# Kernel tuning notes

Measured on AMD Instinct MI355X. Metric: run time of the kernel, lower is better.

Reference implementation:

```python
import jax, jax.numpy as jnp
import numpy as np

CONTEXT_LENGTH = 4096
INPUT_LENGTH = 1024
N_EMBED = 512
HEAD_SIZE = 64
BATCH = 8


def _prefix_causal_mask(T):
    # A=ones(IL,IL), B=zeros(IL,non), C=ones(non,IL), D=tril(non,non)
    il = INPUT_LENGTH
    non = CONTEXT_LENGTH - il
    top = jnp.concatenate([jnp.ones((il, il)), jnp.zeros((il, non))], axis=1)
    bot = jnp.concatenate([jnp.ones((non, il)), jnp.tril(jnp.ones((non, non)))], axis=1)
    E = jnp.concatenate([top, bot], axis=0)
    return E[:T, :T]


def setup_inputs() -> dict:
    key = jax.random.key(0)
    kx, kq, kk, kv = jax.random.split(key, 4)
    scale = N_EMBED ** -0.5
    return {
        "x": jax.random.normal(kx, (BATCH, CONTEXT_LENGTH, N_EMBED), dtype=jnp.float32),
        "Wq": jax.random.normal(kq, (N_EMBED, HEAD_SIZE), dtype=jnp.float32) * scale,
        "Wk": jax.random.normal(kk, (N_EMBED, HEAD_SIZE), dtype=jnp.float32) * scale,
        "Wv": jax.random.normal(kv, (N_EMBED, HEAD_SIZE), dtype=jnp.float32) * scale,
    }


def reference(x, Wq, Wk, Wv):
    B, T, C = x.shape
    q = x @ Wq  # [B,T,h]
    k = x @ Wk  # [B,T,h]
    v = x @ Wv  # [B,T,h]
    # NOTE: original scales by C**-0.5 with C = n_embed (not head_size)
    wei = jnp.einsum("bth,bsh->bts", q, k) * (C ** -0.5)  # [B,T,T]
    mask = _prefix_causal_mask(T)  # [T,T], 1 = visible
    wei = jnp.where(mask == 0, jnp.float32(-jnp.inf), wei)
    wei = jax.nn.softmax(wei, axis=-1)
    # dropout p=0.0 (eval): identity
    return jnp.einsum("bts,bsh->bth", wei, v)  # [B,T,h]
```

## Files before the change

kernel.cpp:

```cpp
#include <hip/hip_runtime.h>
#include <hip/hip_bf16.h>


typedef short short8 __attribute__((ext_vector_type(8)));
typedef float floatx4 __attribute__((ext_vector_type(4)));

static __device__ __forceinline__ unsigned short f2b(float f) {
  unsigned u = __float_as_uint(f);
  unsigned r = (u + 0x7fffu + ((u >> 16) & 1u)) >> 16;
  return (unsigned short)r;
}

static __device__ __forceinline__ unsigned pkbf(float lo, float hi) {
  __hip_bfloat162 t = __float22bfloat162_rn(make_float2(lo, hi));
  unsigned d;
  __builtin_memcpy(&d, &t, 4);
  return d;
}

union S8U {
  short8 s;
  unsigned u[4];
};

__global__ __launch_bounds__(256) void wtrans(
    const float* __restrict__ Wq, const float* __restrict__ Wk,
    const float* __restrict__ Wv, unsigned short* __restrict__ Wtf) {
  int o = blockIdx.x * 256 + threadIdx.x;
  int e = o & 7;
  int ln = (o >> 3) & 63;
  int jg = o >> 9;
  int ks = jg / 12;
  int j = jg % 12;
  int m = j >> 2;
  int n = (j & 3) * 16 + (ln & 15);
  int k = ks * 32 + (ln >> 4) * 8 + e;
  const float* W = (m == 0) ? Wq : (m == 1) ? Wk : Wv;
  Wtf[o] = f2b(W[k * 64 + n]);
}

__global__ __launch_bounds__(256, 3) void proj(
    const float* __restrict__ x, const unsigned short* __restrict__ Wtf,
    unsigned short* __restrict__ q, unsigned short* __restrict__ Kf,
    unsigned short* __restrict__ Vf) {
  __shared__ float Cc[2][12][16][17];

  const int tid = threadIdx.x;
  const int lane = tid & 63;
  const int w = tid >> 6;
  const int u = lane & 15;
  const int qd = lane >> 4;
  const int pr = w >> 1;
  const int p = w & 1;
  const int g0 = blockIdx.x * 32;

  floatx4 acc[12];
#pragma unroll
  for (int j = 0; j < 12; ++j) acc[j] = (floatx4)0.0f;

  const float* xr = x + (size_t)(g0 + pr * 16 + u) * 512;

  for (int it = 0; it < 8; ++it) {
    const int ks = p + it * 2;
    floatx4 x0 = *reinterpret_cast<const floatx4*>(&xr[ks * 32 + qd * 8]);
    floatx4 x1 = *reinterpret_cast<const floatx4*>(&xr[ks * 32 + qd * 8 + 4]);
    S8U a;
    a.u[0] = pkbf(x0[0], x0[1]);
    a.u[1] = pkbf(x0[2], x0[3]);
    a.u[2] = pkbf(x1[0], x1[1]);
    a.u[3] = pkbf(x1[2], x1[3]);
#pragma unroll
    for (int j = 0; j < 12; ++j) {
      short8 bfr = *reinterpret_cast<const short8*>(&Wtf[(size_t)(ks * 12 + j) * 512 + lane * 8]);
      acc[j] = __builtin_amdgcn_mfma_f32_16x16x32_bf16(a.s, bfr, acc[j], 0, 0, 0);
    }
  }

  if (p == 1) {
#pragma unroll
    for (int j = 0; j < 12; ++j)
#pragma unroll
      for (int r = 0; r < 4; ++r)
        Cc[pr][j][qd * 4 + r][u] = acc[j][r];
  }
  __syncthreads();
  if (p == 0) {
#pragma unroll
    for (int j = 0; j < 12; ++j)
#pragma unroll
      for (int r = 0; r < 4; ++r)
        acc[j][r] += Cc[pr][j][qd * 4 + r][u];

    const int rbase = g0 + pr * 16;
    const int b = rbase >> 12;
    const int t = rbase & 4095;
    const int kt = t >> 6;
    const int sb = ((blockIdx.x & 1) << 1) + pr;
    const int sp = blockIdx.x & 1;
    unsigned short* kfb = Kf + ((size_t)(b * 64 + kt)) * 4096;
    unsigned short* vfb = Vf + ((size_t)(b * 64 + kt)) * 4096;

#pragma unroll
    for (int j = 0; j < 4; ++j)
#pragma unroll
      for (int r = 0; r < 4; ++r) {
        q[(size_t)(rbase + qd * 4 + r) * 64 + j * 16 + u] = f2b(acc[j][r]);
        {
          int kh = j >> 1;
          int qd_f = ((j & 1) << 1) + (u >> 3);
          kfb[(size_t)(kh * 4 + sb) * 512 + (qd_f * 16 + (qd * 4 + r)) * 8 + (u & 7)] =
              f2b(acc[4 + j][r]);
        }
        {
          int qd_f = pr * 2 + (qd >> 1);
          int e = ((qd & 1) << 2) + r;
          vfb[(size_t)(sp * 4 + j) * 512 + (qd_f * 16 + u) * 8 + e] = f2b(acc[8 + j][r]);
        }
      }
  }
}

__global__ __launch_bounds__(256, 2) void attn(
    const unsigned short* __restrict__ q, const unsigned short* __restrict__ Kf,
    const unsigned short* __restrict__ Vf, float* __restrict__ out) {
  __shared__ unsigned Pb[4][4][64][4];
  __shared__ float OcA[64][68];
  __shared__ float OcB[64][68];
  __shared__ float Lc[4][64];

  const int tid = threadIdx.x;
  const int lane = tid & 63;
  const int w = tid >> 6;
  const int u = lane & 15;
  const int qd = lane >> 4;

  const int bx = blockIdx.x;
  const int b = bx & 7;
  const int i = bx >> 3;
  const int qt = (i < 32) ? i : (95 - i);
  const int g0 = qt * 64;

  const unsigned short* qp = q + (size_t)b * 4096 * 64;
  const unsigned short* kfp = Kf + (size_t)b * 64 * 4096;
  const unsigned short* vfp = Vf + (size_t)b * 64 * 4096;

  short8 qB[4][2];
#pragma unroll
  for (int nb = 0; nb < 4; ++nb)
#pragma unroll
    for (int kh = 0; kh < 2; ++kh)
      qB[nb][kh] = *reinterpret_cast<const short8*>(
          &qp[(size_t)(g0 + nb * 16 + u) * 64 + kh * 32 + qd * 8]);

  floatx4 OT[4][4];
#pragma unroll
  for (int mb = 0; mb < 4; ++mb)
#pragma unroll
    for (int nb = 0; nb < 4; ++nb) OT[mb][nb] = (floatx4)0.0f;
  float L[4] = {0.f, 0.f, 0.f, 0.f};

  const float cexp = 0.04419417382415922f * 1.4426950408889634f;
  const int ktmax = (qt < 16) ? 15 : qt;

  for (int kt = w; kt <= ktmax; kt += 4) {
    const unsigned short* kb = kfp + (size_t)kt * 4096;
    const unsigned short* vb = vfp + (size_t)kt * 4096;
    short8 kA[8];
#pragma unroll
    for (int f = 0; f < 8; ++f)
      kA[f] = *reinterpret_cast<const short8*>(&kb[(size_t)f * 512 + lane * 8]);
    const bool diag = (qt >= 16) && (kt == qt);

#pragma unroll
    for (int sp = 0; sp < 2; ++sp) {
      short8 vA[4];
#pragma unroll
      for (int mb = 0; mb < 4; ++mb)
        vA[mb] = *reinterpret_cast<const short8*>(
            &vb[(size_t)(sp * 4 + mb) * 512 + lane * 8]);

      floatx4 ST[2][4];
#pragma unroll
      for (int sbb = 0; sbb < 2; ++sbb)
#pragma unroll
        for (int nb = 0; nb < 4; ++nb) ST[sbb][nb] = (floatx4)0.0f;
#pragma unroll
      for (int kh = 0; kh < 2; ++kh)
#pragma unroll
        for (int sbb = 0; sbb < 2; ++sbb)
#pragma unroll
          for (int nb = 0; nb < 4; ++nb)
            ST[sbb][nb] = __builtin_amdgcn_mfma_f32_16x16x32_bf16(
                kA[kh * 4 + sp * 2 + sbb], qB[nb][kh], ST[sbb][nb], 0, 0, 0);

      if (diag) {
#pragma unroll
        for (int sbb = 0; sbb < 2; ++sbb)
#pragma unroll
          for (int nb = 0; nb < 4; ++nb)
#pragma unroll
            for (int r = 0; r < 4; ++r) {
              int sl = (sp * 2 + sbb) * 16 + qd * 4 + r;
              int qr = nb * 16 + u;
              if (sl > qr) ST[sbb][nb][r] = -__builtin_inff();
            }
      }

#pragma unroll
      for (int sbb = 0; sbb < 2; ++sbb)
#pragma unroll
        for (int nb = 0; nb < 4; ++nb) {
#pragma unroll
          for (int r = 0; r < 4; ++r)
            ST[sbb][nb][r] = __builtin_amdgcn_exp2f(ST[sbb][nb][r] * cexp);
          L[nb] += (ST[sbb][nb][0] + ST[sbb][nb][1]) + (ST[sbb][nb][2] + ST[sbb][nb][3]);
          unsigned lo = pkbf(ST[sbb][nb][0], ST[sbb][nb][1]);
          unsigned hi = pkbf(ST[sbb][nb][2], ST[sbb][nb][3]);
          int dl = (sbb * 2 + (qd >> 1)) * 16 + u;
          int d0 = (qd & 1) * 2;
          *reinterpret_cast<uint2*>(&Pb[w][nb][dl][d0]) = make_uint2(lo, hi);
        }

#pragma unroll
      for (int nb = 0; nb < 4; ++nb) {
        short8 pB = *reinterpret_cast<const short8*>(&Pb[w][nb][lane][0]);
#pragma unroll
        for (int mb = 0; mb < 4; ++mb)
          OT[mb][nb] = __builtin_amdgcn_mfma_f32_16x16x32_bf16(vA[mb], pB, OT[mb][nb], 0, 0, 0);
      }
    }
  }

#pragma unroll
  for (int nb = 0; nb < 4; ++nb) {
    L[nb] += __shfl_xor(L[nb], 16);
    L[nb] += __shfl_xor(L[nb], 32);
  }
  if (lane < 16) {
#pragma unroll
    for (int nb = 0; nb < 4; ++nb) Lc[w][nb * 16 + lane] = L[nb];
  }

  if (w == 1) {
#pragma unroll
    for (int mb = 0; mb < 4; ++mb)
#pragma unroll
      for (int nb = 0; nb < 4; ++nb)
        *reinterpret_cast<floatx4*>(&OcA[nb * 16 + u][mb * 16 + qd * 4]) = OT[mb][nb];
  }
  if (w == 3) {
#pragma unroll
    for (int mb = 0; mb < 4; ++mb)
#pragma unroll
      for (int nb = 0; nb < 4; ++nb)
        *reinterpret_cast<floatx4*>(&OcB[nb * 16 + u][mb * 16 + qd * 4]) = OT[mb][nb];
  }
  __syncthreads();
  if (w == 0) {
#pragma unroll
    for (int mb = 0; mb < 4; ++mb)
#pragma unroll
      for (int nb = 0; nb < 4; ++nb)
        OT[mb][nb] += *reinterpret_cast<const floatx4*>(&OcA[nb * 16 + u][mb * 16 + qd * 4]);
  }
  if (w == 2) {
#pragma unroll
    for (int mb = 0; mb < 4; ++mb)
#pragma unroll
      for (int nb = 0; nb < 4; ++nb) {
        OT[mb][nb] += *reinterpret_cast<const floatx4*>(&OcB[nb * 16 + u][mb * 16 + qd * 4]);
        *reinterpret_cast<floatx4*>(&OcB[nb * 16 + u][mb * 16 + qd * 4]) = OT[mb][nb];
      }
  }
  __syncthreads();
  if (w == 0) {
#pragma unroll
    for (int mb = 0; mb < 4; ++mb)
#pragma unroll
      for (int nb = 0; nb < 4; ++nb) {
        OT[mb][nb] += *reinterpret_cast<const floatx4*>(&OcB[nb * 16 + u][mb * 16 + qd * 4]);
        *reinterpret_cast<floatx4*>(&OcA[nb * 16 + u][mb * 16 + qd * 4]) = OT[mb][nb];
      }
  }
  __syncthreads();

  {
    int qr = tid >> 2;
    int h0 = (tid & 3) * 16;
    float Ltot = (Lc[0][qr] + Lc[1][qr]) + (Lc[2][qr] + Lc[3][qr]);
    float inv = 1.0f / Ltot;
    float* op = out + ((size_t)b * 4096 + g0 + qr) * 64 + h0;
#pragma unroll
    for (int c = 0; c < 4; ++c) {
      floatx4 v = *reinterpret_cast<const floatx4*>(&OcA[qr][h0 + c * 4]);
      v *= inv;
      *reinterpret_cast<floatx4*>(&op[c * 4]) = v;
    }
  }
}

extern "C" void kernel_launch(void* const* d_in, const int* in_sizes, int n_in,
                              void* d_out, int out_size, void* d_ws, size_t ws_size,
                              hipStream_t stream) {
  const float* x  = (const float*)d_in[0];
  const float* Wq = (const float*)d_in[1];
  const float* Wk = (const float*)d_in[2];
  const float* Wv = (const float*)d_in[3];

  unsigned short* ws = (unsigned short*)d_ws;
  unsigned short* Wtf = ws;
  unsigned short* qb = ws + 131072;
  unsigned short* kf = qb + 2097152;
  unsigned short* vf = kf + 2097152;

  wtrans<<<384, 256, 0, stream>>>(Wq, Wk, Wv, Wtf);
  proj<<<1024, 256, 0, stream>>>(x, Wtf, qb, kf, vf);
  attn<<<512, 256, 0, stream>>>(qb, kf, vf, (float*)d_out);
}
```

Baseline: 146.8 us.

## Double-buffer K/V register loads in attention and fold softmax scale into Q

The attention loop now prefetches the next K and V tiles into a second register set while computing on the current one, so global-load latency overlaps the MFMA work. The softmax scale and log2e factor are folded into Q at projection time, which removes a multiply per score. The projection kernel also issues all x loads up front before the MFMA loop. The extra register buffers raise VGPR pressure and may lower occupancy under the launch bounds of 2 blocks per SM. Rounding Q after scaling also changes the bf16 values slightly.

```diff
diff --git a/kernel.cpp b/kernel.cpp
--- a/kernel.cpp
+++ b/kernel.cpp
@@ -54,21 +54,28 @@
   const int p = w & 1;
   const int g0 = blockIdx.x * 32;
 
-  floatx4 acc[12];
-#pragma unroll
-  for (int j = 0; j < 12; ++j) acc[j] = (floatx4)0.0f;
-
   const float* xr = x + (size_t)(g0 + pr * 16 + u) * 512;
 
+  floatx4 xv[16];
+#pragma unroll
   for (int it = 0; it < 8; ++it) {
     const int ks = p + it * 2;
-    floatx4 x0 = *reinterpret_cast<const floatx4*>(&xr[ks * 32 + qd * 8]);
-    floatx4 x1 = *reinterpret_cast<const floatx4*>(&xr[ks * 32 + qd * 8 + 4]);
+    xv[it * 2] = *reinterpret_cast<const floatx4*>(&xr[ks * 32 + qd * 8]);
+    xv[it * 2 + 1] = *reinterpret_cast<const floatx4*>(&xr[ks * 32 + qd * 8 + 4]);
+  }
+
+  floatx4 acc[12];
+#pragma unroll
+  for (int j = 0; j < 12; ++j) acc[j] = (floatx4)0.0f;
+
+#pragma unroll
+  for (int it = 0; it < 8; ++it) {
+    const int ks = p + it * 2;
     S8U a;
-    a.u[0] = pkbf(x0[0], x0[1]);
-    a.u[1] = pkbf(x0[2], x0[3]);
-    a.u[2] = pkbf(x1[0], x1[1]);
-    a.u[3] = pkbf(x1[2], x1[3]);
+    a.u[0] = pkbf(xv[it * 2][0], xv[it * 2][1]);
+    a.u[1] = pkbf(xv[it * 2][2], xv[it * 2][3]);
+    a.u[2] = pkbf(xv[it * 2 + 1][0], xv[it * 2 + 1][1]);
+    a.u[3] = pkbf(xv[it * 2 + 1][2], xv[it * 2 + 1][3]);
 #pragma unroll
     for (int j = 0; j < 12; ++j) {
       short8 bfr = *reinterpret_cast<const short8*>(&Wtf[(size_t)(ks * 12 + j) * 512 + lane * 8]);
@@ -91,6 +98,7 @@
       for (int r = 0; r < 4; ++r)
         acc[j][r] += Cc[pr][j][qd * 4 + r][u];
 
+    const float cexp = 0.04419417382415922f * 1.4426950408889634f;
     const int rbase = g0 + pr * 16;
     const int b = rbase >> 12;
     const int t = rbase & 4095;
@@ -104,7 +112,7 @@
     for (int j = 0; j < 4; ++j)
 #pragma unroll
       for (int r = 0; r < 4; ++r) {
-        q[(size_t)(rbase + qd * 4 + r) * 64 + j * 16 + u] = f2b(acc[j][r]);
+        q[(size_t)(rbase + qd * 4 + r) * 64 + j * 16 + u] = f2b(acc[j][r] * cexp);
         {
           int kh = j >> 1;
           int qd_f = ((j & 1) << 1) + (u >> 3);
@@ -159,77 +167,101 @@
     for (int nb = 0; nb < 4; ++nb) OT[mb][nb] = (floatx4)0.0f;
   float L[4] = {0.f, 0.f, 0.f, 0.f};
 
-  const float cexp = 0.04419417382415922f * 1.4426950408889634f;
   const int ktmax = (qt < 16) ? 15 : qt;
 
-  for (int kt = w; kt <= ktmax; kt += 4) {
-    const unsigned short* kb = kfp + (size_t)kt * 4096;
-    const unsigned short* vb = vfp + (size_t)kt * 4096;
-    short8 kA[8];
-#pragma unroll
-    for (int f = 0; f < 8; ++f)
-      kA[f] = *reinterpret_cast<const short8*>(&kb[(size_t)f * 512 + lane * 8]);
-    const bool diag = (qt >= 16) && (kt == qt);
-
-#pragma unroll
-    for (int sp = 0; sp < 2; ++sp) {
-      short8 vA[4];
-#pragma unroll
-      for (int mb = 0; mb < 4; ++mb)
-        vA[mb] = *reinterpret_cast<const short8*>(
-            &vb[(size_t)(sp * 4 + mb) * 512 + lane * 8]);
-
-      floatx4 ST[2][4];
-#pragma unroll
-      for (int sbb = 0; sbb < 2; ++sbb)
-#pragma unroll
-        for (int nb = 0; nb < 4; ++nb) ST[sbb][nb] = (floatx4)0.0f;
-#pragma unroll
-      for (int kh = 0; kh < 2; ++kh)
-#pragma unroll
-        for (int sbb = 0; sbb < 2; ++sbb)
-#pragma unroll
-          for (int nb = 0; nb < 4; ++nb)
-            ST[sbb][nb] = __builtin_amdgcn_mfma_f32_16x16x32_bf16(
-                kA[kh * 4 + sp * 2 + sbb], qB[nb][kh], ST[sbb][nb], 0, 0, 0);
-
-      if (diag) {
-#pragma unroll
-        for (int sbb = 0; sbb < 2; ++sbb)
-#pragma unroll
-          for (int nb = 0; nb < 4; ++nb)
-#pragma unroll
-            for (int r = 0; r < 4; ++r) {
-              int sl = (sp * 2 + sbb) * 16 + qd * 4 + r;
-              int qr = nb * 16 + u;
-              if (sl > qr) ST[sbb][nb][r] = -__builtin_inff();
-            }
-      }
-
-#pragma unroll
-      for (int sbb = 0; sbb < 2; ++sbb)
-#pragma unroll
-        for (int nb = 0; nb < 4; ++nb) {
-#pragma unroll
-          for (int r = 0; r < 4; ++r)
-            ST[sbb][nb][r] = __builtin_amdgcn_exp2f(ST[sbb][nb][r] * cexp);
-          L[nb] += (ST[sbb][nb][0] + ST[sbb][nb][1]) + (ST[sbb][nb][2] + ST[sbb][nb][3]);
-          unsigned lo = pkbf(ST[sbb][nb][0], ST[sbb][nb][1]);
-          unsigned hi = pkbf(ST[sbb][nb][2], ST[sbb][nb][3]);
-          int dl = (sbb * 2 + (qd >> 1)) * 16 + u;
-          int d0 = (qd & 1) * 2;
-          *reinterpret_cast<uint2*>(&Pb[w][nb][dl][d0]) = make_uint2(lo, hi);
-        }
-
-#pragma unroll
-      for (int nb = 0; nb < 4; ++nb) {
-        short8 pB = *reinterpret_cast<const short8*>(&Pb[w][nb][lane][0]);
-#pragma unroll
-        for (int mb = 0; mb < 4; ++mb)
-          OT[mb][nb] = __builtin_amdgcn_mfma_f32_16x16x32_bf16(vA[mb], pB, OT[mb][nb], 0, 0, 0);
-      }
+#define LOADKV(KA, VA, KT)                                                    \
+  do {                                                                        \
+    const unsigned short* kb_ = kfp + (size_t)(KT) * 4096;                    \
+    const unsigned short* vb_ = vfp + (size_t)(KT) * 4096;                    \
+    _Pragma("unroll")                                                         \
+    for (int f = 0; f < 8; ++f) {                                             \
+      KA[f] = *reinterpret_cast<const short8*>(&kb_[(size_t)f * 512 + lane * 8]); \
+      VA[f] = *reinterpret_cast<const short8*>(&vb_[(size_t)f * 512 + lane * 8]); \
+    }                                                                         \
+  } while (0)
+
+#define ATTN_STEP(KA, VA, KT)                                                 \
+  do {                                                                        \
+    const bool diag_ = (qt >= 16) && ((KT) == qt);                            \
+    _Pragma("unroll")                                                         \
+    for (int sp = 0; sp < 2; ++sp) {                                          \
+      floatx4 ST[2][4];                                                       \
+      _Pragma("unroll")                                                       \
+      for (int sbb = 0; sbb < 2; ++sbb)                                       \
+        _Pragma("unroll")                                                     \
+        for (int nb = 0; nb < 4; ++nb) ST[sbb][nb] = (floatx4)0.0f;           \
+      _Pragma("unroll")                                                       \
+      for (int kh = 0; kh < 2; ++kh)                                          \
+        _Pragma("unroll")                                                     \
+        for (int sbb = 0; sbb < 2; ++sbb)                                     \
+          _Pragma("unroll")                                                   \
+          for (int nb = 0; nb < 4; ++nb)                                      \
+            ST[sbb][nb] = __builtin_amdgcn_mfma_f32_16x16x32_bf16(            \
+                KA[kh * 4 + sp * 2 + sbb], qB[nb][kh], ST[sbb][nb], 0, 0, 0); \
+      if (diag_) {                                                            \
+        _Pragma("unroll")                                                     \
+        for (int sbb = 0; sbb < 2; ++sbb)                                     \
+          _Pragma("unroll")                                                   \
+          for (int nb = 0; nb < 4; ++nb)                                      \
+            _Pragma("unroll")                                                 \
+            for (int r = 0; r < 4; ++r) {                                     \
+              int sl = (sp * 2 + sbb) * 16 + qd * 4 + r;                      \
+              int qr = nb * 16 + u;                                           \
+              if (sl > qr) ST[sbb][nb][r] = -__builtin_inff();                \
+            }                                                                 \
+      }                                                                       \
+      _Pragma("unroll")                                                       \
+      for (int sbb = 0; sbb < 2; ++sbb)                                       \
+        _Pragma("unroll")                                                     \
+        for (int nb = 0; nb < 4; ++nb) {                                      \
+          _Pragma("unroll")                                                   \
+          for (int r = 0; r < 4; ++r)                                         \
+            ST[sbb][nb][r] = __builtin_amdgcn_exp2f(ST[sbb][nb][r]);          \
+          L[nb] += (ST[sbb][nb][0] + ST[sbb][nb][1]) +                        \
+                   (ST[sbb][nb][2] + ST[sbb][nb][3]);                         \
+          unsigned lo = pkbf(ST[sbb][nb][0], ST[sbb][nb][1]);                 \
+          unsigned hi = pkbf(ST[sbb][nb][2], ST[sbb][nb][3]);                 \
+          int dl = (sbb * 2 + (qd >> 1)) * 16 + u;                            \
+          int d0 = (qd & 1) * 2;                                              \
+          *reinterpret_cast<uint2*>(&Pb[w][nb][dl][d0]) = make_uint2(lo, hi); \
+        }                                                                     \
+      _Pragma("unroll")                                                       \
+      for (int nb = 0; nb < 4; ++nb) {                                        \
+        short8 pB = *reinterpret_cast<const short8*>(&Pb[w][nb][lane][0]);    \
+        _Pragma("unroll")                                                     \
+        for (int mb = 0; mb < 4; ++mb)                                        \
+          OT[mb][nb] = __builtin_amdgcn_mfma_f32_16x16x32_bf16(               \
+              VA[sp * 4 + mb], pB, OT[mb][nb], 0, 0, 0);                      \
+      }                                                                       \
+    }                                                                         \
+  } while (0)
+
+  short8 kAa[8], vAa[8], kAb[8], vAb[8];
+  LOADKV(kAa, vAa, w);
+  int kt = w;
+  for (;;) {
+    int ktn = kt + 4;
+    if (ktn <= ktmax) {
+      LOADKV(kAb, vAb, ktn);
+      ATTN_STEP(kAa, vAa, kt);
+    } else {
+      ATTN_STEP(kAa, vAa, kt);
+      break;
     }
-  }
+    kt = ktn;
+    ktn = kt + 4;
+    if (ktn <= ktmax) {
+      LOADKV(kAa, vAa, ktn);
+      ATTN_STEP(kAb, vAb, kt);
+    } else {
+      ATTN_STEP(kAb, vAb, kt);
+      break;
+    }
+    kt = ktn;
+  }
+
+#undef LOADKV
+#undef ATTN_STEP
 
 #pragma unroll
   for (int nb = 0; nb < 4; ++nb) {
```

Result: slower. 235.6 us (+60.6%).

## Split attention warps into QK/softmax producers and PV consumers with double-buffered P

Applied to the files above, without the earlier changes.

Warp-specializes the attention kernel: two waves compute QK^T scores and exp, writing bf16 probabilities to a double-buffered shared buffer, while two waves load V and run the PV MFMAs one phase behind, with a block barrier per phase and s_setprio around the MFMA bursts. The softmax scale is folded into q during the projection kernel, which removes one multiply per score. The aim is to overlap exp work with matrix work and reduce reduction traffic at the end. In exchange it adds a __syncthreads every phase, halves the number of waves doing QK work, and quantizes the pre-scaled q to bf16.

```diff
diff --git a/kernel.cpp b/kernel.cpp
--- a/kernel.cpp
+++ b/kernel.cpp
@@ -91,6 +91,7 @@
       for (int r = 0; r < 4; ++r)
         acc[j][r] += Cc[pr][j][qd * 4 + r][u];
 
+    const float cexp = 0.04419417382415922f * 1.4426950408889634f;
     const int rbase = g0 + pr * 16;
     const int b = rbase >> 12;
     const int t = rbase & 4095;
@@ -104,7 +105,7 @@
     for (int j = 0; j < 4; ++j)
 #pragma unroll
       for (int r = 0; r < 4; ++r) {
-        q[(size_t)(rbase + qd * 4 + r) * 64 + j * 16 + u] = f2b(acc[j][r]);
+        q[(size_t)(rbase + qd * 4 + r) * 64 + j * 16 + u] = f2b(acc[j][r] * cexp);
         {
           int kh = j >> 1;
           int qd_f = ((j & 1) << 1) + (u >> 3);
@@ -123,10 +124,9 @@
 __global__ __launch_bounds__(256, 2) void attn(
     const unsigned short* __restrict__ q, const unsigned short* __restrict__ Kf,
     const unsigned short* __restrict__ Vf, float* __restrict__ out) {
-  __shared__ unsigned Pb[4][4][64][4];
+  __shared__ unsigned Pq[2][2][2][4][4][66];
   __shared__ float OcA[64][68];
-  __shared__ float OcB[64][68];
-  __shared__ float Lc[4][64];
+  __shared__ float Lc[2][64];
 
   const int tid = threadIdx.x;
   const int lane = tid & 63;
@@ -144,141 +144,147 @@
   const unsigned short* kfp = Kf + (size_t)b * 64 * 4096;
   const unsigned short* vfp = Vf + (size_t)b * 64 * 4096;
 
+  const int nt = (qt < 16) ? 16 : (qt + 1);
+  const int nph = (nt + 1) >> 1;
+  const bool prod = (w < 2);
+  const int sw = w & 1;
+
   short8 qB[4][2];
-#pragma unroll
-  for (int nb = 0; nb < 4; ++nb)
-#pragma unroll
-    for (int kh = 0; kh < 2; ++kh)
-      qB[nb][kh] = *reinterpret_cast<const short8*>(
-          &qp[(size_t)(g0 + nb * 16 + u) * 64 + kh * 32 + qd * 8]);
+  float L[4] = {0.f, 0.f, 0.f, 0.f};
+  if (prod) {
+#pragma unroll
+    for (int nb = 0; nb < 4; ++nb)
+#pragma unroll
+      for (int kh = 0; kh < 2; ++kh)
+        qB[nb][kh] = *reinterpret_cast<const short8*>(
+            &qp[(size_t)(g0 + nb * 16 + u) * 64 + kh * 32 + qd * 8]);
+  }
 
   floatx4 OT[4][4];
 #pragma unroll
   for (int mb = 0; mb < 4; ++mb)
 #pragma unroll
     for (int nb = 0; nb < 4; ++nb) OT[mb][nb] = (floatx4)0.0f;
-  float L[4] = {0.f, 0.f, 0.f, 0.f};
-
-  const float cexp = 0.04419417382415922f * 1.4426950408889634f;
-  const int ktmax = (qt < 16) ? 15 : qt;
-
-  for (int kt = w; kt <= ktmax; kt += 4) {
-    const unsigned short* kb = kfp + (size_t)kt * 4096;
-    const unsigned short* vb = vfp + (size_t)kt * 4096;
-    short8 kA[8];
-#pragma unroll
-    for (int f = 0; f < 8; ++f)
-      kA[f] = *reinterpret_cast<const short8*>(&kb[(size_t)f * 512 + lane * 8]);
-    const bool diag = (qt >= 16) && (kt == qt);
-
-#pragma unroll
-    for (int sp = 0; sp < 2; ++sp) {
-      short8 vA[4];
-#pragma unroll
-      for (int mb = 0; mb < 4; ++mb)
-        vA[mb] = *reinterpret_cast<const short8*>(
-            &vb[(size_t)(sp * 4 + mb) * 512 + lane * 8]);
-
-      floatx4 ST[2][4];
-#pragma unroll
-      for (int sbb = 0; sbb < 2; ++sbb)
-#pragma unroll
-        for (int nb = 0; nb < 4; ++nb) ST[sbb][nb] = (floatx4)0.0f;
-#pragma unroll
-      for (int kh = 0; kh < 2; ++kh)
-#pragma unroll
-        for (int sbb = 0; sbb < 2; ++sbb)
-#pragma unroll
-          for (int nb = 0; nb < 4; ++nb)
-            ST[sbb][nb] = __builtin_amdgcn_mfma_f32_16x16x32_bf16(
-                kA[kh * 4 + sp * 2 + sbb], qB[nb][kh], ST[sbb][nb], 0, 0, 0);
-
-      if (diag) {
-#pragma unroll
-        for (int sbb = 0; sbb < 2; ++sbb)
-#pragma unroll
-          for (int nb = 0; nb < 4; ++nb)
-#pragma unroll
-            for (int r = 0; r < 4; ++r) {
-              int sl = (sp * 2 + sbb) * 16 + qd * 4 + r;
-              int qr = nb * 16 + u;
-              if (sl > qr) ST[sbb][nb][r] = -__builtin_inff();
+
+  for (int p = 0; p <= nph; ++p) {
+    if (!prod && p > 0) {
+      const int t = (p - 1) * 2 + sw;
+      if (t < nt) {
+        const int rb = (p - 1) & 1;
+        const unsigned short* vb = vfp + (size_t)t * 4096;
+#pragma unroll
+        for (int sp = 0; sp < 2; ++sp) {
+          short8 vA[4];
+#pragma unroll
+          for (int mb = 0; mb < 4; ++mb)
+            vA[mb] = *reinterpret_cast<const short8*>(
+                &vb[(size_t)(sp * 4 + mb) * 512 + lane * 8]);
+#pragma unroll
+          for (int nb = 0; nb < 4; ++nb) {
+            S8U pb;
+#pragma unroll
+            for (int d = 0; d < 4; ++d) pb.u[d] = Pq[rb][sw][sp][nb][d][lane];
+            __builtin_amdgcn_s_setprio(1);
+#pragma unroll
+            for (int mb = 0; mb < 4; ++mb)
+              OT[mb][nb] = __builtin_amdgcn_mfma_f32_16x16x32_bf16(
+                  vA[mb], pb.s, OT[mb][nb], 0, 0, 0);
+            __builtin_amdgcn_s_setprio(0);
+          }
+        }
+      }
+    }
+
+    if (prod && p < nph) {
+      const int t = p * 2 + sw;
+      if (t < nt) {
+        const int wb = p & 1;
+        const unsigned short* kb = kfp + (size_t)t * 4096;
+        short8 kA[8];
+#pragma unroll
+        for (int f = 0; f < 8; ++f)
+          kA[f] = *reinterpret_cast<const short8*>(&kb[(size_t)f * 512 + lane * 8]);
+        const bool diag = (qt >= 16) && (t == nt - 1);
+
+#pragma unroll
+        for (int sp = 0; sp < 2; ++sp) {
+          floatx4 ST[2][4];
+#pragma unroll
+          for (int sbb = 0; sbb < 2; ++sbb)
+#pragma unroll
+            for (int nb = 0; nb < 4; ++nb) ST[sbb][nb] = (floatx4)0.0f;
+
+          __builtin_amdgcn_s_setprio(1);
+#pragma unroll
+          for (int kh = 0; kh < 2; ++kh)
+#pragma unroll
+            for (int sbb = 0; sbb < 2; ++sbb)
+#pragma unroll
+              for (int nb = 0; nb < 4; ++nb)
+                ST[sbb][nb] = __builtin_amdgcn_mfma_f32_16x16x32_bf16(
+                    kA[kh * 4 + sp * 2 + sbb], qB[nb][kh], ST[sbb][nb], 0, 0, 0);
+          __builtin_amdgcn_s_setprio(0);
+
+          if (diag) {
+#pragma unroll
+            for (int sbb = 0; sbb < 2; ++sbb)
+#pragma unroll
+              for (int nb = 0; nb < 4; ++nb)
+#pragma unroll
+                for (int r = 0; r < 4; ++r) {
+                  int sl = (sp * 2 + sbb) * 16 + qd * 4 + r;
+                  int qr = nb * 16 + u;
+                  if (sl > qr) ST[sbb][nb][r] = -__builtin_inff();
+                }
+          }
+
+#pragma unroll
+          for (int sbb = 0; sbb < 2; ++sbb)
+#pragma unroll
+            for (int nb = 0; nb < 4; ++nb) {
+#pragma unroll
+              for (int r = 0; r < 4; ++r)
+                ST[sbb][nb][r] = __builtin_amdgcn_exp2f(ST[sbb][nb][r]);
+              L[nb] += (ST[sbb][nb][0] + ST[sbb][nb][1]) + (ST[sbb][nb][2] + ST[sbb][nb][3]);
+              unsigned lo = pkbf(ST[sbb][nb][0], ST[sbb][nb][1]);
+              unsigned hi = pkbf(ST[sbb][nb][2], ST[sbb][nb][3]);
+              int dl = (sbb * 2 + (qd >> 1)) * 16 + u;
+              int d0 = (qd & 1) * 2;
+              Pq[wb][sw][sp][nb][d0][dl] = lo;
+              Pq[wb][sw][sp][nb][d0 + 1][dl] = hi;
             }
+        }
       }
-
-#pragma unroll
-      for (int sbb = 0; sbb < 2; ++sbb)
-#pragma unroll
-        for (int nb = 0; nb < 4; ++nb) {
-#pragma unroll
-          for (int r = 0; r < 4; ++r)
-            ST[sbb][nb][r] = __builtin_amdgcn_exp2f(ST[sbb][nb][r] * cexp);
-          L[nb] += (ST[sbb][nb][0] + ST[sbb][nb][1]) + (ST[sbb][nb][2] + ST[sbb][nb][3]);
-          unsigned lo = pkbf(ST[sbb][nb][0], ST[sbb][nb][1]);
-          unsigned hi = pkbf(ST[sbb][nb][2], ST[sbb][nb][3]);
-          int dl = (sbb * 2 + (qd >> 1)) * 16 + u;
-          int d0 = (qd & 1) * 2;
-          *reinterpret_cast<uint2*>(&Pb[w][nb][dl][d0]) = make_uint2(lo, hi);
-        }
-
-#pragma unroll
-      for (int nb = 0; nb < 4; ++nb) {
-        short8 pB = *reinterpret_cast<const short8*>(&Pb[w][nb][lane][0]);
-#pragma unroll
-        for (int mb = 0; mb < 4; ++mb)
-          OT[mb][nb] = __builtin_amdgcn_mfma_f32_16x16x32_bf16(vA[mb], pB, OT[mb][nb], 0, 0, 0);
-      }
-    }
-  }
-
-#pragma unroll
-  for (int nb = 0; nb < 4; ++nb) {
-    L[nb] += __shfl_xor(L[nb], 16);
-    L[nb] += __shfl_xor(L[nb], 32);
-  }
-  if (lane < 16) {
-#pragma unroll
-    for (int nb = 0; nb < 4; ++nb) Lc[w][nb * 16 + lane] = L[nb];
-  }
-
-  if (w == 1) {
+    }
+
+    __syncthreads();
+  }
+
+  if (prod) {
+#pragma unroll
+    for (int nb = 0; nb < 4; ++nb) {
+      L[nb] += __shfl_xor(L[nb], 16);
+      L[nb] += __shfl_xor(L[nb], 32);
+    }
+    if (lane < 16) {
+#pragma unroll
+      for (int nb = 0; nb < 4; ++nb) Lc[sw][nb * 16 + lane] = L[nb];
+    }
+  }
+  if (w == 3) {
 #pragma unroll
     for (int mb = 0; mb < 4; ++mb)
 #pragma unroll
       for (int nb = 0; nb < 4; ++nb)
         *reinterpret_cast<floatx4*>(&OcA[nb * 16 + u][mb * 16 + qd * 4]) = OT[mb][nb];
   }
-  if (w == 3) {
+  __syncthreads();
+  if (w == 2) {
 #pragma unroll
     for (int mb = 0; mb < 4; ++mb)
 #pragma unroll
-      for (int nb = 0; nb < 4; ++nb)
-        *reinterpret_cast<floatx4*>(&OcB[nb * 16 + u][mb * 16 + qd * 4]) = OT[mb][nb];
-  }
-  __syncthreads();
-  if (w == 0) {
-#pragma unroll
-    for (int mb = 0; mb < 4; ++mb)
-#pragma unroll
-      for (int nb = 0; nb < 4; ++nb)
+      for (int nb = 0; nb < 4; ++nb) {
         OT[mb][nb] += *reinterpret_cast<const floatx4*>(&OcA[nb * 16 + u][mb * 16 + qd * 4]);
-  }
-  if (w == 2) {
-#pragma unroll
-    for (int mb = 0; mb < 4; ++mb)
-#pragma unroll
-      for (int nb = 0; nb < 4; ++nb) {
-        OT[mb][nb] += *reinterpret_cast<const floatx4*>(&OcB[nb * 16 + u][mb * 16 + qd * 4]);
-        *reinterpret_cast<floatx4*>(&OcB[nb * 16 + u][mb * 16 + qd * 4]) = OT[mb][nb];
-      }
-  }
-  __syncthreads();
-  if (w == 0) {
-#pragma unroll
-    for (int mb = 0; mb < 4; ++mb)
-#pragma unroll
-      for (int nb = 0; nb < 4; ++nb) {
-        OT[mb][nb] += *reinterpret_cast<const floatx4*>(&OcB[nb * 16 + u][mb * 16 + qd * 4]);
         *reinterpret_cast<floatx4*>(&OcA[nb * 16 + u][mb * 16 + qd * 4]) = OT[mb][nb];
       }
   }
@@ -287,7 +293,7 @@
   {
     int qr = tid >> 2;
     int h0 = (tid & 3) * 16;
-    float Ltot = (Lc[0][qr] + Lc[1][qr]) + (Lc[2][qr] + Lc[3][qr]);
+    float Ltot = Lc[0][qr] + Lc[1][qr];
     float inv = 1.0f / Ltot;
     float* op = out + ((size_t)b * 4096 + g0 + qr) * 64 + h0;
 #pragma unroll
```

Result: slower. 163.1 us (+11.1%).

## Split key tiles across eight waves and fold softmax scale into Q

Applied to the files above, without the earlier changes.

The attention kernel now launches 512 threads (8 waves) per block, so each wave handles every eighth key tile, and the cross-wave output reduction becomes a multi-stage tree. Pb and the output-combine buffers share one LDS union. The softmax scale times log2(e) is folded into Q during projection, which removes a multiply per score. MFMA sections are wrapped in s_setprio. The intent is more parallel waves per query tile, which shortens the critical path of long causal tiles. The costs are more barriers in the reduction epilogue, higher register pressure under launch_bounds(512,4), and rounding the pre-scaled Q to bf16.

```diff
diff --git a/kernel.cpp b/kernel.cpp
--- a/kernel.cpp
+++ b/kernel.cpp
@@ -91,6 +91,7 @@
       for (int r = 0; r < 4; ++r)
         acc[j][r] += Cc[pr][j][qd * 4 + r][u];
 
+    const float cexp = 0.04419417382415922f * 1.4426950408889634f;
     const int rbase = g0 + pr * 16;
     const int b = rbase >> 12;
     const int t = rbase & 4095;
@@ -104,7 +105,7 @@
     for (int j = 0; j < 4; ++j)
 #pragma unroll
       for (int r = 0; r < 4; ++r) {
-        q[(size_t)(rbase + qd * 4 + r) * 64 + j * 16 + u] = f2b(acc[j][r]);
+        q[(size_t)(rbase + qd * 4 + r) * 64 + j * 16 + u] = f2b(acc[j][r] * cexp);
         {
           int kh = j >> 1;
           int qd_f = ((j & 1) << 1) + (u >> 3);
@@ -120,13 +121,15 @@
   }
 }
 
-__global__ __launch_bounds__(256, 2) void attn(
+__global__ __launch_bounds__(512, 4) void attn(
     const unsigned short* __restrict__ q, const unsigned short* __restrict__ Kf,
     const unsigned short* __restrict__ Vf, float* __restrict__ out) {
-  __shared__ unsigned Pb[4][4][64][4];
-  __shared__ float OcA[64][68];
-  __shared__ float OcB[64][68];
-  __shared__ float Lc[4][64];
+  union SU {
+    unsigned Pb[8][4][64][4];
+    float Oc[2][64][68];
+  };
+  __shared__ SU sh;
+  __shared__ float Lc[8][64];
 
   const int tid = threadIdx.x;
   const int lane = tid & 63;
@@ -159,10 +162,9 @@
     for (int nb = 0; nb < 4; ++nb) OT[mb][nb] = (floatx4)0.0f;
   float L[4] = {0.f, 0.f, 0.f, 0.f};
 
-  const float cexp = 0.04419417382415922f * 1.4426950408889634f;
   const int ktmax = (qt < 16) ? 15 : qt;
 
-  for (int kt = w; kt <= ktmax; kt += 4) {
+  for (int kt = w; kt <= ktmax; kt += 8) {
     const unsigned short* kb = kfp + (size_t)kt * 4096;
     const unsigned short* vb = vfp + (size_t)kt * 4096;
     short8 kA[8];
@@ -184,6 +186,8 @@
       for (int sbb = 0; sbb < 2; ++sbb)
 #pragma unroll
         for (int nb = 0; nb < 4; ++nb) ST[sbb][nb] = (floatx4)0.0f;
+
+      __builtin_amdgcn_s_setprio(1);
 #pragma unroll
       for (int kh = 0; kh < 2; ++kh)
 #pragma unroll
@@ -192,6 +196,7 @@
           for (int nb = 0; nb < 4; ++nb)
             ST[sbb][nb] = __builtin_amdgcn_mfma_f32_16x16x32_bf16(
                 kA[kh * 4 + sp * 2 + sbb], qB[nb][kh], ST[sbb][nb], 0, 0, 0);
+      __builtin_amdgcn_s_setprio(0);
 
       if (diag) {
 #pragma unroll
@@ -212,22 +217,24 @@
         for (int nb = 0; nb < 4; ++nb) {
 #pragma unroll
           for (int r = 0; r < 4; ++r)
-            ST[sbb][nb][r] = __builtin_amdgcn_exp2f(ST[sbb][nb][r] * cexp);
+            ST[sbb][nb][r] = __builtin_amdgcn_exp2f(ST[sbb][nb][r]);
           L[nb] += (ST[sbb][nb][0] + ST[sbb][nb][1]) + (ST[sbb][nb][2] + ST[sbb][nb][3]);
           unsigned lo = pkbf(ST[sbb][nb][0], ST[sbb][nb][1]);
           unsigned hi = pkbf(ST[sbb][nb][2], ST[sbb][nb][3]);
           int dl = (sbb * 2 + (qd >> 1)) * 16 + u;
           int d0 = (qd & 1) * 2;
-          *reinterpret_cast<uint2*>(&Pb[w][nb][dl][d0]) = make_uint2(lo, hi);
+          *reinterpret_cast<uint2*>(&sh.Pb[w][nb][dl][d0]) = make_uint2(lo, hi);
         }
 
+      __builtin_amdgcn_s_setprio(1);
 #pragma unroll
       for (int nb = 0; nb < 4; ++nb) {
-        short8 pB = *reinterpret_cast<const short8*>(&Pb[w][nb][lane][0]);
+        short8 pB = *reinterpret_cast<const short8*>(&sh.Pb[w][nb][lane][0]);
 #pragma unroll
         for (int mb = 0; mb < 4; ++mb)
           OT[mb][nb] = __builtin_amdgcn_mfma_f32_16x16x32_bf16(vA[mb], pB, OT[mb][nb], 0, 0, 0);
       }
+      __builtin_amdgcn_s_setprio(0);
     }
   }
 
@@ -241,58 +248,63 @@
     for (int nb = 0; nb < 4; ++nb) Lc[w][nb * 16 + lane] = L[nb];
   }
 
-  if (w == 1) {
-#pragma unroll
-    for (int mb = 0; mb < 4; ++mb)
-#pragma unroll
-      for (int nb = 0; nb < 4; ++nb)
-        *reinterpret_cast<floatx4*>(&OcA[nb * 16 + u][mb * 16 + qd * 4]) = OT[mb][nb];
-  }
-  if (w == 3) {
-#pragma unroll
-    for (int mb = 0; mb < 4; ++mb)
-#pragma unroll
-      for (int nb = 0; nb < 4; ++nb)
-        *reinterpret_cast<floatx4*>(&OcB[nb * 16 + u][mb * 16 + qd * 4]) = OT[mb][nb];
-  }
+#define PUBOC(BUF)                                                              \
+  do {                                                                          \
+    _Pragma("unroll")                                                           \
+    for (int mb = 0; mb < 4; ++mb)                                              \
+      _Pragma("unroll")                                                         \
+      for (int nb = 0; nb < 4; ++nb)                                            \
+        *reinterpret_cast<floatx4*>(&sh.Oc[BUF][nb * 16 + u][mb * 16 + qd * 4]) = OT[mb][nb]; \
+  } while (0)
+#define ACCOC(BUF)                                                              \
+  do {                                                                          \
+    _Pragma("unroll")                                                           \
+    for (int mb = 0; mb < 4; ++mb)                                              \
+      _Pragma("unroll")                                                         \
+      for (int nb = 0; nb < 4; ++nb)                                            \
+        OT[mb][nb] += *reinterpret_cast<const floatx4*>(                        \
+            &sh.Oc[BUF][nb * 16 + u][mb * 16 + qd * 4]);                        \
+  } while (0)
+
+  __syncthreads();
+  if (w == 1) PUBOC(0);
+  if (w == 5) PUBOC(1);
+  __syncthreads();
+  if (w == 0) ACCOC(0);
+  if (w == 4) ACCOC(1);
+  __syncthreads();
+  if (w == 3) PUBOC(0);
+  if (w == 7) PUBOC(1);
+  __syncthreads();
+  if (w == 2) ACCOC(0);
+  if (w == 6) ACCOC(1);
+  __syncthreads();
+  if (w == 2) PUBOC(0);
+  if (w == 6) PUBOC(1);
+  __syncthreads();
+  if (w == 0) ACCOC(0);
+  if (w == 4) ACCOC(1);
+  __syncthreads();
+  if (w == 4) PUBOC(0);
   __syncthreads();
   if (w == 0) {
-#pragma unroll
-    for (int mb = 0; mb < 4; ++mb)
-#pragma unroll
-      for (int nb = 0; nb < 4; ++nb)
-        OT[mb][nb] += *reinterpret_cast<const floatx4*>(&OcA[nb * 16 + u][mb * 16 + qd * 4]);
-  }
-  if (w == 2) {
-#pragma unroll
-    for (int mb = 0; mb < 4; ++mb)
-#pragma unroll
-      for (int nb = 0; nb < 4; ++nb) {
-        OT[mb][nb] += *reinterpret_cast<const floatx4*>(&OcB[nb * 16 + u][mb * 16 + qd * 4]);
-        *reinterpret_cast<floatx4*>(&OcB[nb * 16 + u][mb * 16 + qd * 4]) = OT[mb][nb];
-      }
-  }
-  __syncthreads();
-  if (w == 0) {
-#pragma unroll
-    for (int mb = 0; mb < 4; ++mb)
-#pragma unroll
-      for (int nb = 0; nb < 4; ++nb) {
-        OT[mb][nb] += *reinterpret_cast<const floatx4*>(&OcB[nb * 16 + u][mb * 16 + qd * 4]);
-        *reinterpret_cast<floatx4*>(&OcA[nb * 16 + u][mb * 16 + qd * 4]) = OT[mb][nb];
-      }
-  }
-  __syncthreads();
+    ACCOC(0);
+    PUBOC(0);
+  }
+  __syncthreads();
+#undef PUBOC
+#undef ACCOC
 
   {
-    int qr = tid >> 2;
-    int h0 = (tid & 3) * 16;
-    float Ltot = (Lc[0][qr] + Lc[1][qr]) + (Lc[2][qr] + Lc[3][qr]);
+    int qr = tid >> 3;
+    int h0 = (tid & 7) * 8;
+    float Ltot = ((Lc[0][qr] + Lc[1][qr]) + (Lc[2][qr] + Lc[3][qr])) +
+                 ((Lc[4][qr] + Lc[5][qr]) + (Lc[6][qr] + Lc[7][qr]));
     float inv = 1.0f / Ltot;
     float* op = out + ((size_t)b * 4096 + g0 + qr) * 64 + h0;
 #pragma unroll
-    for (int c = 0; c < 4; ++c) {
-      floatx4 v = *reinterpret_cast<const floatx4*>(&OcA[qr][h0 + c * 4]);
+    for (int c = 0; c < 2; ++c) {
+      floatx4 v = *reinterpret_cast<const floatx4*>(&sh.Oc[0][qr][h0 + c * 4]);
       v *= inv;
       *reinterpret_cast<floatx4*>(&op[c * 4]) = v;
     }
@@ -315,5 +327,5 @@
 
   wtrans<<<384, 256, 0, stream>>>(Wq, Wk, Wv, Wtf);
   proj<<<1024, 256, 0, stream>>>(x, Wtf, qb, kf, vf);
-  attn<<<512, 256, 0, stream>>>(qb, kf, vf, (float*)d_out);
-}
+  attn<<<512, 512, 0, stream>>>(qb, kf, vf, (float*)d_out);
+}
```

Measured after the change: 322.7 us. +119.9%, slower.
